# Optimization experiments

Measured on AMD Instinct MI355X. Metric: run time of the kernel, lower is better.

## Reference

```python
import jax, jax.numpy as jnp
import numpy as np

EPS = 1e-12  # matches torch F.normalize default eps


def setup_inputs() -> dict:
    key = jax.random.key(0)
    k_h, = jax.random.split(key, 1)
    B, S, D = 4, 4096, 2048
    h = jax.random.normal(k_h, (B, S, D), dtype=jnp.float32)
    alpha = jnp.asarray(2.0, dtype=jnp.float32)  # alpha_init
    beta = jnp.asarray(0.5, dtype=jnp.float32)   # beta_init
    return {"h": h, "alpha": alpha, "beta": beta}


def reference(h, alpha, beta):
    # --- concentration: mean pairwise cosine similarity (off-diagonal) ---
    # F.normalize(h, dim=-1): x / max(||x||_2, eps)
    norm = jnp.linalg.norm(h, axis=-1, keepdims=True)
    h_norm = h / jnp.maximum(norm, EPS)
    # sim: (B, S, S) via batched GEMM, same as torch.bmm
    sim = jnp.einsum('bid,bjd->bij', h_norm, h_norm)
    B, S, _ = sim.shape
    # mean over all off-diagonal entries across the whole batch
    diag_sum = jnp.einsum('bii->', sim)
    denom = jnp.asarray(B * S * (S - 1), dtype=sim.dtype)
    conc = (jnp.sum(sim) - diag_sum) / denom
    lambda_t = jax.nn.sigmoid(alpha * (conc - beta))
    return (lambda_t, conc)
```

## Files before the change

### kernel.cpp

```cpp
#include <hip/hip_runtime.h>
#include <math.h>

#define NBATCH 4
#define SROWS  4096
#define DCOLS  2048
#define BPB    128
#define NBLK1  (NBATCH * BPB)
#define ROWS_PER_WAVE (SROWS / (BPB * 4))

#define SSQ_OFFSET ((size_t)NBLK1 * DCOLS)

__global__ __launch_bounds__(256, 2)
void row_normalize_sum(const float* __restrict__ h, float* __restrict__ part) {
    const int b    = blockIdx.x >> 7;
    const int blk  = blockIdx.x & (BPB - 1);
    const int wave = threadIdx.x >> 6;
    const int lane = threadIdx.x & 63;

    const float* hb = h + (size_t)b * SROWS * DCOLS;
    const int wid      = blk * 4 + wave;
    const int row_base = wid * ROWS_PER_WAVE;

    float acc[32];
#pragma unroll
    for (int i = 0; i < 32; ++i) acc[i] = 0.0f;

    for (int r = 0; r < ROWS_PER_WAVE; r += 2) {
        const float4* p0 = (const float4*)(hb + (size_t)(row_base + r)     * DCOLS) + lane;
        const float4* p1 = (const float4*)(hb + (size_t)(row_base + r + 1) * DCOLS) + lane;
        float4 v0[8], v1[8];
#pragma unroll
        for (int s = 0; s < 8; ++s) v0[s] = p0[s * 64];
#pragma unroll
        for (int s = 0; s < 8; ++s) v1[s] = p1[s * 64];

        float ss0 = 0.0f, ss1 = 0.0f;
#pragma unroll
        for (int s = 0; s < 8; ++s) {
            ss0 += v0[s].x * v0[s].x + v0[s].y * v0[s].y + v0[s].z * v0[s].z + v0[s].w * v0[s].w;
            ss1 += v1[s].x * v1[s].x + v1[s].y * v1[s].y + v1[s].z * v1[s].z + v1[s].w * v1[s].w;
        }
#pragma unroll
        for (int m = 32; m >= 1; m >>= 1) {
            ss0 += __shfl_xor(ss0, m, 64);
            ss1 += __shfl_xor(ss1, m, 64);
        }
        const float inv0 = (float)(1.0 / fmax(sqrt((double)ss0), 1e-12));
        const float inv1 = (float)(1.0 / fmax(sqrt((double)ss1), 1e-12));
#pragma unroll
        for (int s = 0; s < 8; ++s) {
            acc[s * 4 + 0] += v0[s].x * inv0;
            acc[s * 4 + 1] += v0[s].y * inv0;
            acc[s * 4 + 2] += v0[s].z * inv0;
            acc[s * 4 + 3] += v0[s].w * inv0;
            acc[s * 4 + 0] += v1[s].x * inv1;
            acc[s * 4 + 1] += v1[s].y * inv1;
            acc[s * 4 + 2] += v1[s].z * inv1;
            acc[s * 4 + 3] += v1[s].w * inv1;
        }
    }

    __shared__ float red[4][DCOLS];
#pragma unroll
    for (int s = 0; s < 8; ++s) {
        float4* dst = (float4*)&red[wave][s * 256 + lane * 4];
        *dst = make_float4(acc[s * 4 + 0], acc[s * 4 + 1], acc[s * 4 + 2], acc[s * 4 + 3]);
    }
    __syncthreads();

    float* dst = part + (size_t)blockIdx.x * DCOLS;
#pragma unroll
    for (int k = 0; k < 8; ++k) {
        const int c = k * 256 + threadIdx.x;
        dst[c] = red[0][c] + red[1][c] + red[2][c] + red[3][c];
    }
}

__global__ __launch_bounds__(256, 4)
void reduce_partials(const float* __restrict__ part, double* __restrict__ ssq_part) {
    const int b    = blockIdx.x >> 4;
    const int c    = ((blockIdx.x & 15) * 128) + (threadIdx.x & 127);
    const int half = threadIdx.x >> 7;
    const float* pb = part + (size_t)b * BPB * DCOLS;

    double sum = 0.0;
    const int p0 = half * 64;
#pragma unroll 8
    for (int p = p0; p < p0 + 64; ++p)
        sum += (double)pb[(size_t)p * DCOLS + c];

    __shared__ double sh[256];
    sh[threadIdx.x] = sum;
    __syncthreads();

    double ssq = 0.0;
    if (threadIdx.x < 128) {
        const double s = sh[threadIdx.x] + sh[threadIdx.x + 128];
        ssq = s * s;
    }
    __syncthreads();
    sh[threadIdx.x] = ssq;
    __syncthreads();
    for (int off = 64; off > 0; off >>= 1) {
        if (threadIdx.x < off) sh[threadIdx.x] += sh[threadIdx.x + off];
        __syncthreads();
    }
    if (threadIdx.x == 0) ssq_part[blockIdx.x] = sh[0];
}

__global__ void finalize_kernel(const double* __restrict__ ssq_part,
                                const float* __restrict__ alpha,
                                const float* __restrict__ beta,
                                float* __restrict__ out) {
    double v = ssq_part[threadIdx.x];
#pragma unroll
    for (int m = 32; m >= 1; m >>= 1) v += __shfl_xor(v, m, 64);
    if (threadIdx.x == 0) {
        const double num   = v - (double)NBATCH * (double)SROWS;
        const double denom = (double)NBATCH * (double)SROWS * (double)(SROWS - 1);
        const double conc  = num / denom;
        const double a  = (double)alpha[0];
        const double bt = (double)beta[0];
        const double lam = 1.0 / (1.0 + exp(-a * (conc - bt)));
        out[0] = (float)lam;
        out[1] = (float)conc;
    }
}

extern "C" void kernel_launch(void* const* d_in, const int* in_sizes, int n_in,
                              void* d_out, int out_size, void* d_ws, size_t ws_size,
                              hipStream_t stream) {
    (void)in_sizes; (void)n_in; (void)out_size; (void)ws_size;
    const float* h     = (const float*)d_in[0];
    const float* alpha = (const float*)d_in[1];
    const float* beta  = (const float*)d_in[2];
    float* out         = (float*)d_out;
    float* part        = (float*)d_ws;
    double* ssq_part   = (double*)((float*)d_ws + SSQ_OFFSET);

    row_normalize_sum<<<NBLK1, 256, 0, stream>>>(h, part);
    reduce_partials<<<64, 256, 0, stream>>>(part, ssq_part);
    finalize_kernel<<<1, 64, 0, stream>>>(ssq_part, alpha, beta, out);
}
```

Measured before the change: 199.9 us.

## Fuse finalize into reduction via last-block atomic counter; use nontemporal loads

Merges the finalize kernel into the partial-reduction kernel: each block publishes its partial with a release store and bumps an atomic counter, and the last block does the final reduction and sigmoid. The counter is reset by the first kernel. Input loads are switched to nontemporal builtins so the 128 MB streaming read does not pollute the cache. This removes one kernel launch at the cost of atomics and an extra per-block synchronisation.

Result: faster. 187.6 us (median of 2 runs) (-6.2%).

```diff
diff --git a/kernel.cpp b/kernel.cpp
--- a/kernel.cpp
+++ b/kernel.cpp
@@ -10,8 +10,13 @@
 
 #define SSQ_OFFSET ((size_t)NBLK1 * DCOLS)
 
+typedef float v4f __attribute__((ext_vector_type(4)));
+
 __global__ __launch_bounds__(256, 2)
-void row_normalize_sum(const float* __restrict__ h, float* __restrict__ part) {
+void row_normalize_sum(const float* __restrict__ h, float* __restrict__ part,
+                       unsigned* __restrict__ counter) {
+    if (blockIdx.x == 0 && threadIdx.x == 0) *counter = 0u;
+
     const int b    = blockIdx.x >> 7;
     const int blk  = blockIdx.x & (BPB - 1);
     const int wave = threadIdx.x >> 6;
@@ -26,19 +31,22 @@
     for (int i = 0; i < 32; ++i) acc[i] = 0.0f;
 
     for (int r = 0; r < ROWS_PER_WAVE; r += 2) {
-        const float4* p0 = (const float4*)(hb + (size_t)(row_base + r)     * DCOLS) + lane;
-        const float4* p1 = (const float4*)(hb + (size_t)(row_base + r + 1) * DCOLS) + lane;
-        float4 v0[8], v1[8];
+        const v4f* p0 = (const v4f*)(hb + (size_t)(row_base + r)     * DCOLS) + lane;
+        const v4f* p1 = (const v4f*)(hb + (size_t)(row_base + r + 1) * DCOLS) + lane;
+        v4f v0[8], v1[8];
 #pragma unroll
-        for (int s = 0; s < 8; ++s) v0[s] = p0[s * 64];
+        for (int s = 0; s < 8; ++s) v0[s] = __builtin_nontemporal_load(p0 + s * 64);
 #pragma unroll
-        for (int s = 0; s < 8; ++s) v1[s] = p1[s * 64];
+        for (int s = 0; s < 8; ++s) v1[s] = __builtin_nontemporal_load(p1 + s * 64);
 
         float ss0 = 0.0f, ss1 = 0.0f;
 #pragma unroll
         for (int s = 0; s < 8; ++s) {
-            ss0 += v0[s].x * v0[s].x + v0[s].y * v0[s].y + v0[s].z * v0[s].z + v0[s].w * v0[s].w;
-            ss1 += v1[s].x * v1[s].x + v1[s].y * v1[s].y + v1[s].z * v1[s].z + v1[s].w * v1[s].w;
+#pragma unroll
+            for (int j = 0; j < 4; ++j) {
+                ss0 += v0[s][j] * v0[s][j];
+                ss1 += v1[s][j] * v1[s][j];
+            }
         }
 #pragma unroll
         for (int m = 32; m >= 1; m >>= 1) {
@@ -49,22 +57,21 @@
         const float inv1 = (float)(1.0 / fmax(sqrt((double)ss1), 1e-12));
 #pragma unroll
         for (int s = 0; s < 8; ++s) {
-            acc[s * 4 + 0] += v0[s].x * inv0;
-            acc[s * 4 + 1] += v0[s].y * inv0;
-            acc[s * 4 + 2] += v0[s].z * inv0;
-            acc[s * 4 + 3] += v0[s].w * inv0;
-            acc[s * 4 + 0] += v1[s].x * inv1;
-            acc[s * 4 + 1] += v1[s].y * inv1;
-            acc[s * 4 + 2] += v1[s].z * inv1;
-            acc[s * 4 + 3] += v1[s].w * inv1;
+#pragma unroll
+            for (int j = 0; j < 4; ++j) {
+                acc[s * 4 + j] += v0[s][j] * inv0;
+                acc[s * 4 + j] += v1[s][j] * inv1;
+            }
         }
     }
 
     __shared__ float red[4][DCOLS];
 #pragma unroll
     for (int s = 0; s < 8; ++s) {
-        float4* dst = (float4*)&red[wave][s * 256 + lane * 4];
-        *dst = make_float4(acc[s * 4 + 0], acc[s * 4 + 1], acc[s * 4 + 2], acc[s * 4 + 3]);
+        v4f v;
+#pragma unroll
+        for (int j = 0; j < 4; ++j) v[j] = acc[s * 4 + j];
+        *(v4f*)&red[wave][s * 256 + lane * 4] = v;
     }
     __syncthreads();
 
@@ -77,16 +84,21 @@
 }
 
 __global__ __launch_bounds__(256, 4)
-void reduce_partials(const float* __restrict__ part, double* __restrict__ ssq_part) {
+void reduce_partials_finalize(const float* __restrict__ part,
+                              double* __restrict__ ssq_part,
+                              unsigned* __restrict__ counter,
+                              const float* __restrict__ alpha,
+                              const float* __restrict__ beta,
+                              float* __restrict__ out) {
     const int b    = blockIdx.x >> 4;
     const int c    = ((blockIdx.x & 15) * 128) + (threadIdx.x & 127);
     const int half = threadIdx.x >> 7;
     const float* pb = part + (size_t)b * BPB * DCOLS;
 
     double sum = 0.0;
-    const int p0 = half * 64;
-#pragma unroll 8
-    for (int p = p0; p < p0 + 64; ++p)
+    const int pstart = half * 64;
+#pragma unroll 16
+    for (int p = pstart; p < pstart + 64; ++p)
         sum += (double)pb[(size_t)p * DCOLS + c];
 
     __shared__ double sh[256];
@@ -95,8 +107,8 @@
 
     double ssq = 0.0;
     if (threadIdx.x < 128) {
-        const double s = sh[threadIdx.x] + sh[threadIdx.x + 128];
-        ssq = s * s;
+        const double s2 = sh[threadIdx.x] + sh[threadIdx.x + 128];
+        ssq = s2 * s2;
     }
     __syncthreads();
     sh[threadIdx.x] = ssq;
@@ -105,25 +117,32 @@
         if (threadIdx.x < off) sh[threadIdx.x] += sh[threadIdx.x + off];
         __syncthreads();
     }
-    if (threadIdx.x == 0) ssq_part[blockIdx.x] = sh[0];
-}
 
-__global__ void finalize_kernel(const double* __restrict__ ssq_part,
-                                const float* __restrict__ alpha,
-                                const float* __restrict__ beta,
-                                float* __restrict__ out) {
-    double v = ssq_part[threadIdx.x];
+    __shared__ int lastFlag;
+    if (threadIdx.x == 0) {
+        __hip_atomic_store(&ssq_part[blockIdx.x], sh[0],
+                           __ATOMIC_RELEASE, __HIP_MEMORY_SCOPE_AGENT);
+        const unsigned t = __hip_atomic_fetch_add(counter, 1u,
+                           __ATOMIC_ACQ_REL, __HIP_MEMORY_SCOPE_AGENT);
+        lastFlag = (t == 63u) ? 1 : 0;
+    }
+    __syncthreads();
+
+    if (lastFlag && threadIdx.x < 64) {
+        double v = __hip_atomic_load(&ssq_part[threadIdx.x],
+                                     __ATOMIC_ACQUIRE, __HIP_MEMORY_SCOPE_AGENT);
 #pragma unroll
-    for (int m = 32; m >= 1; m >>= 1) v += __shfl_xor(v, m, 64);
-    if (threadIdx.x == 0) {
-        const double num   = v - (double)NBATCH * (double)SROWS;
-        const double denom = (double)NBATCH * (double)SROWS * (double)(SROWS - 1);
-        const double conc  = num / denom;
-        const double a  = (double)alpha[0];
-        const double bt = (double)beta[0];
-        const double lam = 1.0 / (1.0 + exp(-a * (conc - bt)));
-        out[0] = (float)lam;
-        out[1] = (float)conc;
+        for (int m = 32; m >= 1; m >>= 1) v += __shfl_xor(v, m, 64);
+        if (threadIdx.x == 0) {
+            const double num   = v - (double)NBATCH * (double)SROWS;
+            const double denom = (double)NBATCH * (double)SROWS * (double)(SROWS - 1);
+            const double conc  = num / denom;
+            const double a  = (double)alpha[0];
+            const double bt = (double)beta[0];
+            const double lam = 1.0 / (1.0 + exp(-a * (conc - bt)));
+            out[0] = (float)lam;
+            out[1] = (float)conc;
+        }
     }
 }
 
@@ -137,8 +156,9 @@
     float* out         = (float*)d_out;
     float* part        = (float*)d_ws;
     double* ssq_part   = (double*)((float*)d_ws + SSQ_OFFSET);
+    unsigned* counter  = (unsigned*)(ssq_part + 64);
 
-    row_normalize_sum<<<NBLK1, 256, 0, stream>>>(h, part);
-    reduce_partials<<<64, 256, 0, stream>>>(part, ssq_part);
-    finalize_kernel<<<1, 64, 0, stream>>>(ssq_part, alpha, beta, out);
+    row_normalize_sum<<<NBLK1, 256, 0, stream>>>(h, part, counter);
+    reduce_partials_finalize<<<64, 256, 0, stream>>>(part, ssq_part, counter,
+                                                     alpha, beta, out);
 }
```
